# Kernel tuning notes

Measured on AMD Instinct MI355X. Metric: run time of the kernel, lower is better.

## Reference

```python
import jax, jax.numpy as jnp
import numpy as np

SQRT_2PI = (2.0 * 3.14159) ** 0.5  # matches torch.jit.script gaussian constant


def setup_inputs() -> dict:
    key = jax.random.key(0)
    ks = jax.random.split(key, 7)
    B, N, R, K, H, HEADS = 4, 256, 4, 128, 512, 32
    rpe = jax.random.uniform(ks[0], (B, N, N, R), dtype=jnp.float32) * 5.0
    means = jax.random.uniform(ks[1], (R, K), dtype=jnp.float32, minval=0.0, maxval=3.0)
    stds = jax.random.uniform(ks[2], (R, K), dtype=jnp.float32, minval=0.0, maxval=3.0)
    W1 = jax.random.normal(ks[3], (H, R * K), dtype=jnp.float32) * (1.0 / (R * K) ** 0.5)
    b1 = jax.random.normal(ks[4], (H,), dtype=jnp.float32) * 0.01
    W2 = jax.random.normal(ks[5], (HEADS, H), dtype=jnp.float32) * (1.0 / H ** 0.5)
    b2 = jax.random.normal(ks[6], (HEADS,), dtype=jnp.float32) * 0.01
    return {"rpe": rpe, "means": means, "stds": stds, "W1": W1, "b1": b1, "W2": W2, "b2": b2}


def reference(rpe, means, stds, W1, b1, W2, b2):
    # GaussianLayer: (B,N,N,R) -> (B,N,N,R*K)
    std = jnp.abs(stds) + 0.01                      # (R,K)
    x = rpe[..., None]                              # (B,N,N,R,1)
    g = jnp.exp(-0.5 * ((x - means) / std) ** 2) / (SQRT_2PI * std)  # (B,N,N,R,K)
    B, N = rpe.shape[0], rpe.shape[1]
    g = g.reshape(B, N, N, -1)                      # (B,N,N,R*K)
    # NonLinear MLP: Linear -> gelu(exact) -> Linear
    h = jax.nn.gelu(jnp.einsum('bmnf,hf->bmnh', g, W1) + b1, approximate=False)
    out = jnp.einsum('bmnh,oh->bmno', h, W2) + b2   # (B,N,N,heads)
    # permute BATCH_HEAD_NODE_NODE = (0,3,1,2)
    return jnp.transpose(out, (0, 3, 1, 2))
```

## Files before the change

### kernel.cpp

```cpp
#include <hip/hip_runtime.h>
#include <hip/hip_bf16.h>

typedef __attribute__((ext_vector_type(8))) short bfrag8;
typedef __attribute__((ext_vector_type(4))) float f32x4;
typedef __attribute__((ext_vector_type(4))) unsigned int u32x4;

#define IS2_SCALE 0.84932180028801907f
#define W1_SCALE  0.46971724f

#if __has_builtin(__builtin_amdgcn_exp2f)
#define GEXP(x) __builtin_amdgcn_exp2f(x)
#else
__device__ __forceinline__ float gexp_asm(float x) {
  float r; asm("v_exp_f32 %0, %1" : "=v"(r) : "v"(x)); return r;
}
#define GEXP(x) gexp_asm(x)
#endif

__device__ __forceinline__ unsigned short f2bf(float x) {
  union { float f; unsigned u; } v; v.f = x;
  unsigned r = v.u + 0x7fffu + ((v.u >> 16) & 1u);
  return (unsigned short)(r >> 16);
}
__device__ __forceinline__ unsigned cvtpk(float lo, float hi) {
  unsigned r;
  asm("v_cvt_pk_bf16_f32 %0, %1, %2" : "=v"(r) : "v"(lo), "v"(hi));
  return r;
}
__device__ __forceinline__ float rcpa(float x) {
  float r; asm("v_rcp_f32 %0, %1" : "=v"(r) : "v"(x)); return r;
}
__device__ __forceinline__ float gelu_fast(float x) {
  float x2 = x * x;
  float w = __builtin_fmaf(x2, -0.1029488f, -2.3022078f);
  float e = GEXP(x * w);
  return x * rcpa(e + 1.0f);
}

__device__ __forceinline__ void gauss_frags(const f32x4* prm4, const f32x4 xa, const f32x4 xb,
                                            int kb, int lg, bfrag8* A0, bfrag8* A1) {
  const int k0 = kb * 32 + lg * 8;
  const float x0 = xa[kb >> 2], x1 = xb[kb >> 2];
  unsigned pk0[4], pk1[4];
#pragma unroll
  for (int q = 0; q < 4; ++q) {
    f32x4 P = prm4[(k0 >> 1) + q];
    float u00 = __builtin_fmaf(x0, P[1], P[0]);
    float u01 = __builtin_fmaf(x0, P[3], P[2]);
    float u10 = __builtin_fmaf(x1, P[1], P[0]);
    float u11 = __builtin_fmaf(x1, P[3], P[2]);
    pk0[q] = cvtpk(P[1] * GEXP(-(u00 * u00)), P[3] * GEXP(-(u01 * u01)));
    pk1[q] = cvtpk(P[1] * GEXP(-(u10 * u10)), P[3] * GEXP(-(u11 * u11)));
  }
  u32x4 av0 = {pk0[0], pk0[1], pk0[2], pk0[3]};
  u32x4 av1 = {pk1[0], pk1[1], pk1[2], pk1[3]};
  *A0 = __builtin_bit_cast(bfrag8, av0);
  *A1 = __builtin_bit_cast(bfrag8, av1);
}

__global__ void prep_kernel(const float* __restrict__ means, const float* __restrict__ stds,
                            const float* __restrict__ W1, const float* __restrict__ W2,
                            unsigned short* __restrict__ W1bf, unsigned short* __restrict__ W2bf,
                            float* __restrict__ prm ) {
  int t = blockIdx.x * blockDim.x + threadIdx.x;
  int stride = gridDim.x * blockDim.x;
  for (int i = t; i < 512 * 512; i += stride) W1bf[i] = f2bf(W1[i] * W1_SCALE);
  for (int i = t; i < 32 * 512; i += stride) W2bf[i] = f2bf(W2[i]);
  for (int i = t; i < 512; i += stride) {
    float s = fabsf(stds[i]) + 0.01f;
    float is2 = (1.0f / s) * IS2_SCALE;
    prm[2 * i] = -means[i] * is2;
    prm[2 * i + 1] = is2;
  }
}

__global__ __launch_bounds__(1024, 4) void fused_kernel(
    const float* __restrict__ rpe, const unsigned short* __restrict__ W1bf,
    const unsigned short* __restrict__ W2bf, const float* __restrict__ prm,
    const float* __restrict__ b1, const float* __restrict__ b2,
    float* __restrict__ out) {
  __shared__ __attribute__((aligned(16))) char lds[131072 + 4096 + 2048 + 2048];
  char*  gsl   = lds + 98304;
  float* prm_s = (float*)(lds + 131072);
  float* rpe_s = (float*)(lds + 131072 + 4096);
  float* b1_s  = (float*)(lds + 131072 + 4096 + 2048);

  const int tid = threadIdx.x;
  const int rb = blockIdx.x * 128;

  if (tid < 512) rpe_s[tid] = rpe[rb * 4 + tid];
  prm_s[tid] = prm[tid];
  if (tid < 512) b1_s[tid] = b1[tid];

  int goff[2];
#pragma unroll
  for (int i = 0; i < 2; ++i) {
    int c = i * 1024 + tid;
    int j = ((c >> 6) << 4) + (c & 15);
    goff[i] = j * 512 + ((c >> 4) & 3) * 8;
  }
  const char* Wc = (const char*)W1bf;

#define STAGE(buf, kb)                                                          \
  {                                                                             \
    _Pragma("unroll") for (int i_ = 0; i_ < 2; ++i_) {                          \
      const void* gp = (const void*)(Wc + (size_t)goff[i_] * 2 + (kb) * 64);    \
      void* lp = (void*)(lds + (buf) * 32768 + i_ * 16384 + tid * 16);          \
      __builtin_amdgcn_global_load_lds(                                         \
          (const __attribute__((address_space(1))) void*)gp,                    \
          (__attribute__((address_space(3))) void*)lp, 16, 0, 0);               \
    }                                                                           \
  }

  STAGE(0, 0);
  STAGE(1, 1);

  const int w = tid >> 6, l = tid & 63;
  const int lr = l & 15, lg = l >> 4;
  const int mw = w >> 2, nw = w & 3;
  const int r0 = mw * 32 + lr;
  const bool prod = (mw == nw);

  const f32x4 xa = *(const f32x4*)&rpe_s[r0 * 4];
  const f32x4 xb = *(const f32x4*)&rpe_s[(r0 + 16) * 4];
  const f32x4* prm4 = (const f32x4*)prm_s;

  char* gbase = gsl + mw * 2048 + lg * 256 + lr * 16;

  __syncthreads();

  if (prod) {
    bfrag8 t0, t1;
    gauss_frags(prm4, xa, xb, 0, lg, &t0, &t1);
    *(bfrag8*)(gbase) = t0;  *(bfrag8*)(gbase + 1024) = t1;
    gauss_frags(prm4, xa, xb, 1, lg, &t0, &t1);
    *(bfrag8*)(gbase + 8192) = t0;  *(bfrag8*)(gbase + 8192 + 1024) = t1;
  }
  __syncthreads();

  f32x4 zv = {0.f, 0.f, 0.f, 0.f};
  f32x4 acc[2][8];
#pragma unroll
  for (int mf = 0; mf < 2; ++mf)
#pragma unroll
    for (int nf = 0; nf < 8; ++nf) acc[mf][nf] = zv;

  bfrag8 acur0 = *(const bfrag8*)(gbase);
  bfrag8 acur1 = *(const bfrag8*)(gbase + 1024);
  bfrag8 fA[4], fB[4];
  {
    const char* Bb = lds + nw * 8192 + lg * 256 + lr * 16;
#pragma unroll
    for (int nf = 0; nf < 4; ++nf) fA[nf] = *(const bfrag8*)(Bb + nf * 1024);
  }

#pragma unroll
  for (int kb = 0; kb < 16; ++kb) {
    asm volatile("s_waitcnt vmcnt(0)" ::: "memory");
    __builtin_amdgcn_s_barrier();
    __builtin_amdgcn_sched_barrier(0);
    if (kb < 14) STAGE((kb + 2) % 3, kb + 2);

    const char* Bb = lds + (kb % 3) * 32768 + nw * 8192 + lg * 256 + lr * 16;
    __builtin_amdgcn_s_setprio(1);
#pragma unroll
    for (int nf = 0; nf < 4; ++nf) fB[nf] = *(const bfrag8*)(Bb + (nf + 4) * 1024);
#pragma unroll
    for (int nf = 0; nf < 4; ++nf) {
      acc[0][nf] = __builtin_amdgcn_mfma_f32_16x16x32_bf16(acur0, fA[nf], acc[0][nf], 0, 0, 0);
      acc[1][nf] = __builtin_amdgcn_mfma_f32_16x16x32_bf16(acur1, fA[nf], acc[1][nf], 0, 0, 0);
    }
    __builtin_amdgcn_s_setprio(0);
    __builtin_amdgcn_sched_barrier(0);

    __builtin_amdgcn_s_setprio(1);
    if (kb < 15) {
      const char* Bn = lds + ((kb + 1) % 3) * 32768 + nw * 8192 + lg * 256 + lr * 16;
#pragma unroll
      for (int nf = 0; nf < 4; ++nf) fA[nf] = *(const bfrag8*)(Bn + nf * 1024);
    }
#pragma unroll
    for (int nf = 0; nf < 4; ++nf) {
      acc[0][nf + 4] = __builtin_amdgcn_mfma_f32_16x16x32_bf16(acur0, fB[nf], acc[0][nf + 4], 0, 0, 0);
      acc[1][nf + 4] = __builtin_amdgcn_mfma_f32_16x16x32_bf16(acur1, fB[nf], acc[1][nf + 4], 0, 0, 0);
    }
    __builtin_amdgcn_s_setprio(0);

    if (kb < 15) {
      const char* gs = gbase + ((kb + 1) % 3) * 8192;
      acur0 = *(const bfrag8*)(gs);
      acur1 = *(const bfrag8*)(gs + 1024);
    }
    if (prod && kb < 14) {
      bfrag8 t0, t1;
      gauss_frags(prm4, xa, xb, kb + 2, lg, &t0, &t1);
      char* gd = gbase + ((kb + 2) % 3) * 8192;
      *(bfrag8*)(gd) = t0;  *(bfrag8*)(gd + 1024) = t1;
      asm volatile("s_waitcnt lgkmcnt(0)" ::: "memory");
    }
    __builtin_amdgcn_sched_barrier(0);
  }
  __syncthreads();

  unsigned short* hbuf = (unsigned short*)lds;
#pragma unroll
  for (int mf = 0; mf < 2; ++mf) {
#pragma unroll
    for (int nf = 0; nf < 8; nf += 2) {
      int col0 = nw * 128 + nf * 16 + lr;
      int col1 = col0 + 16;
      float bb0 = b1_s[col0], bb1 = b1_s[col1];
#pragma unroll
      for (int bi = 0; bi < 4; ++bi) {
        float g0 = gelu_fast(acc[mf][nf][bi] + bb0);
        float g1 = gelu_fast(acc[mf][nf + 1][bi] + bb1);
        unsigned pr = cvtpk(g0, g1);
        int hrow = mw * 32 + mf * 16 + lg * 4 + bi;
        int base = hrow * 1024, sw = (hrow & 7) << 4;
        *(unsigned short*)((char*)hbuf + base + ((col0 * 2) ^ sw)) = (unsigned short)pr;
        *(unsigned short*)((char*)hbuf + base + ((col1 * 2) ^ sw)) = (unsigned short)(pr >> 16);
      }
    }
  }
  __syncthreads();

  const int rt = w >> 1, ct = w & 1;
  f32x4 acc2 = zv;
  const int row2 = rt * 16 + lr;
  for (int kb = 0; kb < 16; ++kb) {
    int cb = (kb * 64 + lg * 16) ^ ((row2 & 7) << 4);
    bfrag8 a = *(const bfrag8*)((char*)hbuf + row2 * 1024 + cb);
    bfrag8 b = *(const bfrag8*)(W2bf + (size_t)(ct * 16 + lr) * 512 + kb * 32 + lg * 8);
    acc2 = __builtin_amdgcn_mfma_f32_16x16x32_bf16(a, b, acc2, 0, 0, 0);
  }
  float b2v = b2[ct * 16 + lr];
  __syncthreads();

  float* ob = (float*)lds;
#pragma unroll
  for (int bi = 0; bi < 4; ++bi)
    ob[(rt * 16 + lg * 4 + bi) * 33 + (ct * 16 + lr)] = acc2[bi] + b2v;
  __syncthreads();

  const int bI = rb >> 16, mI = (rb >> 8) & 255, n0 = rb & 255;
  float* obase = out + ((size_t)(bI * 32) * 256 + mI) * 256 + n0;
#pragma unroll
  for (int p = 0; p < 4; ++p) {
    int e = tid + p * 1024;
    int o = e >> 7, i = e & 127;
    obase[(size_t)o * 65536 + i] = ob[i * 33 + o];
  }
#undef STAGE
}

extern "C" void kernel_launch(void* const* d_in, const int* in_sizes, int n_in,
                              void* d_out, int out_size, void* d_ws, size_t ws_size,
                              hipStream_t stream) {
  const float* rpe   = (const float*)d_in[0];
  const float* means = (const float*)d_in[1];
  const float* stds  = (const float*)d_in[2];
  const float* W1    = (const float*)d_in[3];
  const float* b1    = (const float*)d_in[4];
  const float* W2    = (const float*)d_in[5];
  const float* b2    = (const float*)d_in[6];
  float* out = (float*)d_out;

  char* ws = (char*)d_ws;
  unsigned short* W1bf = (unsigned short*)ws;
  unsigned short* W2bf = (unsigned short*)(ws + 524288);
  float* prm = (float*)(ws + 557056);

  prep_kernel<<<256, 256, 0, stream>>>(means, stds, W1, W2, W1bf, W2bf, prm);
  fused_kernel<<<2048, 1024, 0, stream>>>(rpe, W1bf, W2bf, prm, b1, b2, out);
}
```

Before: 257.4 us.

## Process two row tiles per block, prefetching next tile's W1 during epilogue

Halves the grid so each block handles two 128-row tiles in a loop. The first W1 stages and rpe values for the second tile are issued during the first tile's second GEMM and output epilogue. The output staging buffer moves to the gaussian region so it does not clash with the prefetched W1 buffers. This aims to hide pipeline fill and launch/prologue cost, at the expense of fewer blocks and less parallelism across CUs.

New measurement: 486.0 us. +88.8%, slower.

```diff
diff --git a/kernel.cpp b/kernel.cpp
--- a/kernel.cpp
+++ b/kernel.cpp
@@ -86,9 +86,8 @@
   float* b1_s  = (float*)(lds + 131072 + 4096 + 2048);
 
   const int tid = threadIdx.x;
-  const int rb = blockIdx.x * 128;
-
-  if (tid < 512) rpe_s[tid] = rpe[rb * 4 + tid];
+
+  if (tid < 512) rpe_s[tid] = rpe[(size_t)blockIdx.x * 1024 + tid];
   prm_s[tid] = prm[tid];
   if (tid < 512) b1_s[tid] = b1[tid];
 
@@ -114,6 +113,7 @@
 
   STAGE(0, 0);
   STAGE(1, 1);
+  __syncthreads();
 
   const int w = tid >> 6, l = tid & 63;
   const int lr = l & 15, lg = l >> 4;
@@ -121,134 +121,144 @@
   const int r0 = mw * 32 + lr;
   const bool prod = (mw == nw);
 
-  const f32x4 xa = *(const f32x4*)&rpe_s[r0 * 4];
-  const f32x4 xb = *(const f32x4*)&rpe_s[(r0 + 16) * 4];
   const f32x4* prm4 = (const f32x4*)prm_s;
-
   char* gbase = gsl + mw * 2048 + lg * 256 + lr * 16;
-
-  __syncthreads();
-
-  if (prod) {
-    bfrag8 t0, t1;
-    gauss_frags(prm4, xa, xb, 0, lg, &t0, &t1);
-    *(bfrag8*)(gbase) = t0;  *(bfrag8*)(gbase + 1024) = t1;
-    gauss_frags(prm4, xa, xb, 1, lg, &t0, &t1);
-    *(bfrag8*)(gbase + 8192) = t0;  *(bfrag8*)(gbase + 8192 + 1024) = t1;
-  }
-  __syncthreads();
-
   f32x4 zv = {0.f, 0.f, 0.f, 0.f};
-  f32x4 acc[2][8];
-#pragma unroll
-  for (int mf = 0; mf < 2; ++mf)
-#pragma unroll
-    for (int nf = 0; nf < 8; ++nf) acc[mf][nf] = zv;
-
-  bfrag8 acur0 = *(const bfrag8*)(gbase);
-  bfrag8 acur1 = *(const bfrag8*)(gbase + 1024);
-  bfrag8 fA[4], fB[4];
-  {
-    const char* Bb = lds + nw * 8192 + lg * 256 + lr * 16;
-#pragma unroll
-    for (int nf = 0; nf < 4; ++nf) fA[nf] = *(const bfrag8*)(Bb + nf * 1024);
-  }
-
-#pragma unroll
-  for (int kb = 0; kb < 16; ++kb) {
-    asm volatile("s_waitcnt vmcnt(0)" ::: "memory");
-    __builtin_amdgcn_s_barrier();
-    __builtin_amdgcn_sched_barrier(0);
-    if (kb < 14) STAGE((kb + 2) % 3, kb + 2);
-
-    const char* Bb = lds + (kb % 3) * 32768 + nw * 8192 + lg * 256 + lr * 16;
-    __builtin_amdgcn_s_setprio(1);
-#pragma unroll
-    for (int nf = 0; nf < 4; ++nf) fB[nf] = *(const bfrag8*)(Bb + (nf + 4) * 1024);
-#pragma unroll
-    for (int nf = 0; nf < 4; ++nf) {
-      acc[0][nf] = __builtin_amdgcn_mfma_f32_16x16x32_bf16(acur0, fA[nf], acc[0][nf], 0, 0, 0);
-      acc[1][nf] = __builtin_amdgcn_mfma_f32_16x16x32_bf16(acur1, fA[nf], acc[1][nf], 0, 0, 0);
-    }
-    __builtin_amdgcn_s_setprio(0);
-    __builtin_amdgcn_sched_barrier(0);
-
-    __builtin_amdgcn_s_setprio(1);
-    if (kb < 15) {
-      const char* Bn = lds + ((kb + 1) % 3) * 32768 + nw * 8192 + lg * 256 + lr * 16;
-#pragma unroll
-      for (int nf = 0; nf < 4; ++nf) fA[nf] = *(const bfrag8*)(Bn + nf * 1024);
-    }
-#pragma unroll
-    for (int nf = 0; nf < 4; ++nf) {
-      acc[0][nf + 4] = __builtin_amdgcn_mfma_f32_16x16x32_bf16(acur0, fB[nf], acc[0][nf + 4], 0, 0, 0);
-      acc[1][nf + 4] = __builtin_amdgcn_mfma_f32_16x16x32_bf16(acur1, fB[nf], acc[1][nf + 4], 0, 0, 0);
-    }
-    __builtin_amdgcn_s_setprio(0);
-
-    if (kb < 15) {
-      const char* gs = gbase + ((kb + 1) % 3) * 8192;
-      acur0 = *(const bfrag8*)(gs);
-      acur1 = *(const bfrag8*)(gs + 1024);
-    }
-    if (prod && kb < 14) {
-      bfrag8 t0, t1;
-      gauss_frags(prm4, xa, xb, kb + 2, lg, &t0, &t1);
-      char* gd = gbase + ((kb + 2) % 3) * 8192;
-      *(bfrag8*)(gd) = t0;  *(bfrag8*)(gd + 1024) = t1;
-      asm volatile("s_waitcnt lgkmcnt(0)" ::: "memory");
-    }
-    __builtin_amdgcn_sched_barrier(0);
-  }
-  __syncthreads();
-
-  unsigned short* hbuf = (unsigned short*)lds;
-#pragma unroll
-  for (int mf = 0; mf < 2; ++mf) {
-#pragma unroll
-    for (int nf = 0; nf < 8; nf += 2) {
-      int col0 = nw * 128 + nf * 16 + lr;
-      int col1 = col0 + 16;
-      float bb0 = b1_s[col0], bb1 = b1_s[col1];
-#pragma unroll
-      for (int bi = 0; bi < 4; ++bi) {
-        float g0 = gelu_fast(acc[mf][nf][bi] + bb0);
-        float g1 = gelu_fast(acc[mf][nf + 1][bi] + bb1);
-        unsigned pr = cvtpk(g0, g1);
-        int hrow = mw * 32 + mf * 16 + lg * 4 + bi;
-        int base = hrow * 1024, sw = (hrow & 7) << 4;
-        *(unsigned short*)((char*)hbuf + base + ((col0 * 2) ^ sw)) = (unsigned short)pr;
-        *(unsigned short*)((char*)hbuf + base + ((col1 * 2) ^ sw)) = (unsigned short)(pr >> 16);
-      }
-    }
-  }
-  __syncthreads();
-
-  const int rt = w >> 1, ct = w & 1;
-  f32x4 acc2 = zv;
-  const int row2 = rt * 16 + lr;
-  for (int kb = 0; kb < 16; ++kb) {
-    int cb = (kb * 64 + lg * 16) ^ ((row2 & 7) << 4);
-    bfrag8 a = *(const bfrag8*)((char*)hbuf + row2 * 1024 + cb);
-    bfrag8 b = *(const bfrag8*)(W2bf + (size_t)(ct * 16 + lr) * 512 + kb * 32 + lg * 8);
-    acc2 = __builtin_amdgcn_mfma_f32_16x16x32_bf16(a, b, acc2, 0, 0, 0);
-  }
-  float b2v = b2[ct * 16 + lr];
-  __syncthreads();
-
-  float* ob = (float*)lds;
-#pragma unroll
-  for (int bi = 0; bi < 4; ++bi)
-    ob[(rt * 16 + lg * 4 + bi) * 33 + (ct * 16 + lr)] = acc2[bi] + b2v;
-  __syncthreads();
-
-  const int bI = rb >> 16, mI = (rb >> 8) & 255, n0 = rb & 255;
-  float* obase = out + ((size_t)(bI * 32) * 256 + mI) * 256 + n0;
-#pragma unroll
-  for (int p = 0; p < 4; ++p) {
-    int e = tid + p * 1024;
-    int o = e >> 7, i = e & 127;
-    obase[(size_t)o * 65536 + i] = ob[i * 33 + o];
+
+#pragma unroll 1
+  for (int t = 0; t < 2; ++t) {
+    const int rb = blockIdx.x * 256 + t * 128;
+
+    const f32x4 xa = *(const f32x4*)&rpe_s[r0 * 4];
+    const f32x4 xb = *(const f32x4*)&rpe_s[(r0 + 16) * 4];
+
+    if (prod) {
+      bfrag8 t0f, t1f;
+      gauss_frags(prm4, xa, xb, 0, lg, &t0f, &t1f);
+      *(bfrag8*)(gbase) = t0f;  *(bfrag8*)(gbase + 1024) = t1f;
+      gauss_frags(prm4, xa, xb, 1, lg, &t0f, &t1f);
+      *(bfrag8*)(gbase + 8192) = t0f;  *(bfrag8*)(gbase + 8192 + 1024) = t1f;
+    }
+    __syncthreads();
+
+    f32x4 acc[2][8];
+#pragma unroll
+    for (int mf = 0; mf < 2; ++mf)
+#pragma unroll
+      for (int nf = 0; nf < 8; ++nf) acc[mf][nf] = zv;
+
+    bfrag8 acur0 = *(const bfrag8*)(gbase);
+    bfrag8 acur1 = *(const bfrag8*)(gbase + 1024);
+    bfrag8 fA[4], fB[4];
+    {
+      const char* Bb = lds + nw * 8192 + lg * 256 + lr * 16;
+#pragma unroll
+      for (int nf = 0; nf < 4; ++nf) fA[nf] = *(const bfrag8*)(Bb + nf * 1024);
+    }
+
+#pragma unroll
+    for (int kb = 0; kb < 16; ++kb) {
+      asm volatile("s_waitcnt vmcnt(0)" ::: "memory");
+      __builtin_amdgcn_s_barrier();
+      __builtin_amdgcn_sched_barrier(0);
+      if (kb < 14) STAGE((kb + 2) % 3, kb + 2);
+
+      const char* Bb = lds + (kb % 3) * 32768 + nw * 8192 + lg * 256 + lr * 16;
+      __builtin_amdgcn_s_setprio(1);
+#pragma unroll
+      for (int nf = 0; nf < 4; ++nf) fB[nf] = *(const bfrag8*)(Bb + (nf + 4) * 1024);
+#pragma unroll
+      for (int nf = 0; nf < 4; ++nf) {
+        acc[0][nf] = __builtin_amdgcn_mfma_f32_16x16x32_bf16(acur0, fA[nf], acc[0][nf], 0, 0, 0);
+        acc[1][nf] = __builtin_amdgcn_mfma_f32_16x16x32_bf16(acur1, fA[nf], acc[1][nf], 0, 0, 0);
+      }
+      __builtin_amdgcn_s_setprio(0);
+      __builtin_amdgcn_sched_barrier(0);
+
+      __builtin_amdgcn_s_setprio(1);
+      if (kb < 15) {
+        const char* Bn = lds + ((kb + 1) % 3) * 32768 + nw * 8192 + lg * 256 + lr * 16;
+#pragma unroll
+        for (int nf = 0; nf < 4; ++nf) fA[nf] = *(const bfrag8*)(Bn + nf * 1024);
+      }
+#pragma unroll
+      for (int nf = 0; nf < 4; ++nf) {
+        acc[0][nf + 4] = __builtin_amdgcn_mfma_f32_16x16x32_bf16(acur0, fB[nf], acc[0][nf + 4], 0, 0, 0);
+        acc[1][nf + 4] = __builtin_amdgcn_mfma_f32_16x16x32_bf16(acur1, fB[nf], acc[1][nf + 4], 0, 0, 0);
+      }
+      __builtin_amdgcn_s_setprio(0);
+
+      if (kb < 15) {
+        const char* gs = gbase + ((kb + 1) % 3) * 8192;
+        acur0 = *(const bfrag8*)(gs);
+        acur1 = *(const bfrag8*)(gs + 1024);
+      }
+      if (prod && kb < 14) {
+        bfrag8 t0f, t1f;
+        gauss_frags(prm4, xa, xb, kb + 2, lg, &t0f, &t1f);
+        char* gd = gbase + ((kb + 2) % 3) * 8192;
+        *(bfrag8*)(gd) = t0f;  *(bfrag8*)(gd + 1024) = t1f;
+        asm volatile("s_waitcnt lgkmcnt(0)" ::: "memory");
+      }
+      __builtin_amdgcn_sched_barrier(0);
+    }
+    __syncthreads();
+
+    unsigned short* hbuf = (unsigned short*)lds;
+#pragma unroll
+    for (int mf = 0; mf < 2; ++mf) {
+#pragma unroll
+      for (int nf = 0; nf < 8; nf += 2) {
+        int col0 = nw * 128 + nf * 16 + lr;
+        int col1 = col0 + 16;
+        float bb0 = b1_s[col0], bb1 = b1_s[col1];
+#pragma unroll
+        for (int bi = 0; bi < 4; ++bi) {
+          float g0 = gelu_fast(acc[mf][nf][bi] + bb0);
+          float g1 = gelu_fast(acc[mf][nf + 1][bi] + bb1);
+          unsigned pr = cvtpk(g0, g1);
+          int hrow = mw * 32 + mf * 16 + lg * 4 + bi;
+          int base = hrow * 1024, sw = (hrow & 7) << 4;
+          *(unsigned short*)((char*)hbuf + base + ((col0 * 2) ^ sw)) = (unsigned short)pr;
+          *(unsigned short*)((char*)hbuf + base + ((col1 * 2) ^ sw)) = (unsigned short)(pr >> 16);
+        }
+      }
+    }
+    __syncthreads();
+
+    const int rt = w >> 1, ct = w & 1;
+    f32x4 acc2 = zv;
+    const int row2 = rt * 16 + lr;
+    for (int kb = 0; kb < 16; ++kb) {
+      int cb = (kb * 64 + lg * 16) ^ ((row2 & 7) << 4);
+      bfrag8 a = *(const bfrag8*)((char*)hbuf + row2 * 1024 + cb);
+      bfrag8 b = *(const bfrag8*)(W2bf + (size_t)(ct * 16 + lr) * 512 + kb * 32 + lg * 8);
+      acc2 = __builtin_amdgcn_mfma_f32_16x16x32_bf16(a, b, acc2, 0, 0, 0);
+    }
+    float b2v = b2[ct * 16 + lr];
+    __syncthreads();
+
+    if (t == 0) {
+      STAGE(0, 0);
+      STAGE(1, 1);
+      if (tid < 512) rpe_s[tid] = rpe[((size_t)blockIdx.x * 2 + 1) * 512 + tid];
+    }
+
+    float* ob = (float*)gsl;
+#pragma unroll
+    for (int bi = 0; bi < 4; ++bi)
+      ob[(rt * 16 + lg * 4 + bi) * 33 + (ct * 16 + lr)] = acc2[bi] + b2v;
+    __syncthreads();
+
+    const int bI = rb >> 16, mI = (rb >> 8) & 255, n0 = rb & 255;
+    float* obase = out + ((size_t)(bI * 32) * 256 + mI) * 256 + n0;
+#pragma unroll
+    for (int p = 0; p < 4; ++p) {
+      int e = tid + p * 1024;
+      int o = e >> 7, i = e & 127;
+      obase[(size_t)o * 65536 + i] = ob[i * 33 + o];
+    }
+    if (t == 0) __syncthreads();
   }
 #undef STAGE
 }
@@ -271,5 +281,5 @@
   float* prm = (float*)(ws + 557056);
 
   prep_kernel<<<256, 256, 0, stream>>>(means, stds, W1, W2, W1bf, W2bf, prm);
-  fused_kernel<<<2048, 1024, 0, stream>>>(rpe, W1bf, W2bf, prm, b1, b2, out);
-}
+  fused_kernel<<<1024, 1024, 0, stream>>>(rpe, W1bf, W2bf, prm, b1, b2, out);
+}
```

## Remap GEMM1 warp tiling to 2x8 grid with 64x64 per-wave tiles

Applied to the files above, without the earlier changes.

Changes the 16-wave layout for the first GEMM from 4x4 waves (32 rows x 128 cols each) to 2x8 waves (64 rows x 64 cols each). Each wave now holds four A fragments and two B fragments per half-step instead of two A and four B. The Gaussian producer waves become waves 0, 5, 10 and 15, each writing its 32-row slice. This shifts the balance of LDS fragment reads between the A and B operands and spreads the producer work across different SIMDs, which may change LDS traffic and bank pressure.

Result: no change. 258.6 us (+0.5%).

```diff
diff --git a/kernel.cpp b/kernel.cpp
--- a/kernel.cpp
+++ b/kernel.cpp
@@ -117,41 +117,42 @@
 
   const int w = tid >> 6, l = tid & 63;
   const int lr = l & 15, lg = l >> 4;
-  const int mw = w >> 2, nw = w & 3;
-  const int r0 = mw * 32 + lr;
-  const bool prod = (mw == nw);
-
-  const f32x4 xa = *(const f32x4*)&rpe_s[r0 * 4];
-  const f32x4 xb = *(const f32x4*)&rpe_s[(r0 + 16) * 4];
+  const int mw = w >> 3, nw = w & 7;
+  const bool prod = (w % 5 == 0);
+  const int pw = w / 5;
+
+  const f32x4 xpa = *(const f32x4*)&rpe_s[(pw * 32 + lr) * 4];
+  const f32x4 xpb = *(const f32x4*)&rpe_s[(pw * 32 + 16 + lr) * 4];
   const f32x4* prm4 = (const f32x4*)prm_s;
 
-  char* gbase = gsl + mw * 2048 + lg * 256 + lr * 16;
+  char* gwr = gsl + (2 * pw) * 1024 + lg * 256 + lr * 16;
+  const char* grd = gsl + (mw * 4) * 1024 + lg * 256 + lr * 16;
 
   __syncthreads();
 
   if (prod) {
     bfrag8 t0, t1;
-    gauss_frags(prm4, xa, xb, 0, lg, &t0, &t1);
-    *(bfrag8*)(gbase) = t0;  *(bfrag8*)(gbase + 1024) = t1;
-    gauss_frags(prm4, xa, xb, 1, lg, &t0, &t1);
-    *(bfrag8*)(gbase + 8192) = t0;  *(bfrag8*)(gbase + 8192 + 1024) = t1;
+    gauss_frags(prm4, xpa, xpb, 0, lg, &t0, &t1);
+    *(bfrag8*)(gwr) = t0;  *(bfrag8*)(gwr + 1024) = t1;
+    gauss_frags(prm4, xpa, xpb, 1, lg, &t0, &t1);
+    *(bfrag8*)(gwr + 8192) = t0;  *(bfrag8*)(gwr + 8192 + 1024) = t1;
   }
   __syncthreads();
 
   f32x4 zv = {0.f, 0.f, 0.f, 0.f};
-  f32x4 acc[2][8];
-#pragma unroll
-  for (int mf = 0; mf < 2; ++mf)
-#pragma unroll
-    for (int nf = 0; nf < 8; ++nf) acc[mf][nf] = zv;
-
-  bfrag8 acur0 = *(const bfrag8*)(gbase);
-  bfrag8 acur1 = *(const bfrag8*)(gbase + 1024);
-  bfrag8 fA[4], fB[4];
+  f32x4 acc[4][4];
+#pragma unroll
+  for (int rf = 0; rf < 4; ++rf)
+#pragma unroll
+    for (int cf = 0; cf < 4; ++cf) acc[rf][cf] = zv;
+
+  bfrag8 a[4], fA[2], fB[2];
+#pragma unroll
+  for (int rf = 0; rf < 4; ++rf) a[rf] = *(const bfrag8*)(grd + rf * 1024);
   {
-    const char* Bb = lds + nw * 8192 + lg * 256 + lr * 16;
-#pragma unroll
-    for (int nf = 0; nf < 4; ++nf) fA[nf] = *(const bfrag8*)(Bb + nf * 1024);
+    const char* Bb = lds + (nw * 4) * 1024 + lg * 256 + lr * 16;
+    fA[0] = *(const bfrag8*)(Bb);
+    fA[1] = *(const bfrag8*)(Bb + 1024);
   }
 
 #pragma unroll
@@ -161,40 +162,41 @@
     __builtin_amdgcn_sched_barrier(0);
     if (kb < 14) STAGE((kb + 2) % 3, kb + 2);
 
-    const char* Bb = lds + (kb % 3) * 32768 + nw * 8192 + lg * 256 + lr * 16;
+    const char* Bb = lds + (kb % 3) * 32768 + (nw * 4) * 1024 + lg * 256 + lr * 16;
+
     __builtin_amdgcn_s_setprio(1);
-#pragma unroll
-    for (int nf = 0; nf < 4; ++nf) fB[nf] = *(const bfrag8*)(Bb + (nf + 4) * 1024);
-#pragma unroll
-    for (int nf = 0; nf < 4; ++nf) {
-      acc[0][nf] = __builtin_amdgcn_mfma_f32_16x16x32_bf16(acur0, fA[nf], acc[0][nf], 0, 0, 0);
-      acc[1][nf] = __builtin_amdgcn_mfma_f32_16x16x32_bf16(acur1, fA[nf], acc[1][nf], 0, 0, 0);
+    fB[0] = *(const bfrag8*)(Bb + 2048);
+    fB[1] = *(const bfrag8*)(Bb + 3072);
+#pragma unroll
+    for (int rf = 0; rf < 4; ++rf) {
+      acc[rf][0] = __builtin_amdgcn_mfma_f32_16x16x32_bf16(a[rf], fA[0], acc[rf][0], 0, 0, 0);
+      acc[rf][1] = __builtin_amdgcn_mfma_f32_16x16x32_bf16(a[rf], fA[1], acc[rf][1], 0, 0, 0);
     }
     __builtin_amdgcn_s_setprio(0);
     __builtin_amdgcn_sched_barrier(0);
 
     __builtin_amdgcn_s_setprio(1);
     if (kb < 15) {
-      const char* Bn = lds + ((kb + 1) % 3) * 32768 + nw * 8192 + lg * 256 + lr * 16;
-#pragma unroll
-      for (int nf = 0; nf < 4; ++nf) fA[nf] = *(const bfrag8*)(Bn + nf * 1024);
-    }
-#pragma unroll
-    for (int nf = 0; nf < 4; ++nf) {
-      acc[0][nf + 4] = __builtin_amdgcn_mfma_f32_16x16x32_bf16(acur0, fB[nf], acc[0][nf + 4], 0, 0, 0);
-      acc[1][nf + 4] = __builtin_amdgcn_mfma_f32_16x16x32_bf16(acur1, fB[nf], acc[1][nf + 4], 0, 0, 0);
+      const char* Bn = lds + ((kb + 1) % 3) * 32768 + (nw * 4) * 1024 + lg * 256 + lr * 16;
+      fA[0] = *(const bfrag8*)(Bn);
+      fA[1] = *(const bfrag8*)(Bn + 1024);
+    }
+#pragma unroll
+    for (int rf = 0; rf < 4; ++rf) {
+      acc[rf][2] = __builtin_amdgcn_mfma_f32_16x16x32_bf16(a[rf], fB[0], acc[rf][2], 0, 0, 0);
+      acc[rf][3] = __builtin_amdgcn_mfma_f32_16x16x32_bf16(a[rf], fB[1], acc[rf][3], 0, 0, 0);
     }
     __builtin_amdgcn_s_setprio(0);
 
     if (kb < 15) {
-      const char* gs = gbase + ((kb + 1) % 3) * 8192;
-      acur0 = *(const bfrag8*)(gs);
-      acur1 = *(const bfrag8*)(gs + 1024);
+      const char* gs = grd + ((kb + 1) % 3) * 8192;
+#pragma unroll
+      for (int rf = 0; rf < 4; ++rf) a[rf] = *(const bfrag8*)(gs + rf * 1024);
     }
     if (prod && kb < 14) {
       bfrag8 t0, t1;
-      gauss_frags(prm4, xa, xb, kb + 2, lg, &t0, &t1);
-      char* gd = gbase + ((kb + 2) % 3) * 8192;
+      gauss_frags(prm4, xpa, xpb, kb + 2, lg, &t0, &t1);
+      char* gd = gwr + ((kb + 2) % 3) * 8192;
       *(bfrag8*)(gd) = t0;  *(bfrag8*)(gd + 1024) = t1;
       asm volatile("s_waitcnt lgkmcnt(0)" ::: "memory");
     }
@@ -204,18 +206,18 @@
 
   unsigned short* hbuf = (unsigned short*)lds;
 #pragma unroll
-  for (int mf = 0; mf < 2; ++mf) {
-#pragma unroll
-    for (int nf = 0; nf < 8; nf += 2) {
-      int col0 = nw * 128 + nf * 16 + lr;
+  for (int rf = 0; rf < 4; ++rf) {
+#pragma unroll
+    for (int cf = 0; cf < 4; cf += 2) {
+      int col0 = nw * 64 + cf * 16 + lr;
       int col1 = col0 + 16;
       float bb0 = b1_s[col0], bb1 = b1_s[col1];
 #pragma unroll
       for (int bi = 0; bi < 4; ++bi) {
-        float g0 = gelu_fast(acc[mf][nf][bi] + bb0);
-        float g1 = gelu_fast(acc[mf][nf + 1][bi] + bb1);
+        float g0 = gelu_fast(acc[rf][cf][bi] + bb0);
+        float g1 = gelu_fast(acc[rf][cf + 1][bi] + bb1);
         unsigned pr = cvtpk(g0, g1);
-        int hrow = mw * 32 + mf * 16 + lg * 4 + bi;
+        int hrow = mw * 64 + rf * 16 + lg * 4 + bi;
         int base = hrow * 1024, sw = (hrow & 7) << 4;
         *(unsigned short*)((char*)hbuf + base + ((col0 * 2) ^ sw)) = (unsigned short)pr;
         *(unsigned short*)((char*)hbuf + base + ((col1 * 2) ^ sw)) = (unsigned short)(pr >> 16);
@@ -229,9 +231,9 @@
   const int row2 = rt * 16 + lr;
   for (int kb = 0; kb < 16; ++kb) {
     int cb = (kb * 64 + lg * 16) ^ ((row2 & 7) << 4);
-    bfrag8 a = *(const bfrag8*)((char*)hbuf + row2 * 1024 + cb);
+    bfrag8 a2 = *(const bfrag8*)((char*)hbuf + row2 * 1024 + cb);
     bfrag8 b = *(const bfrag8*)(W2bf + (size_t)(ct * 16 + lr) * 512 + kb * 32 + lg * 8);
-    acc2 = __builtin_amdgcn_mfma_f32_16x16x32_bf16(a, b, acc2, 0, 0, 0);
+    acc2 = __builtin_amdgcn_mfma_f32_16x16x32_bf16(a2, b, acc2, 0, 0, 0);
   }
   float b2v = b2[ct * 16 + lr];
   __syncthreads();
```
